# Optimization experiments

Hardware: AMD Instinct MI355X
Metric: run time of the kernel (lower is better)

Reference implementation:

```python
import jax, jax.numpy as jnp
import numpy as np

B, S, IN_DIM, HID = 8, 2048, 1024, 1024


def setup_inputs() -> dict:
    key = jax.random.key(0)
    k1, k2, k3, k4, k5 = jax.random.split(key, 5)
    vec = jax.random.normal(k1, (B, S, IN_DIM), dtype=jnp.float32)
    # nn.Linear-style init scale
    wq_w = jax.random.normal(k2, (HID, IN_DIM), dtype=jnp.float32) / np.sqrt(IN_DIM)
    wq_b = jax.random.normal(k3, (HID,), dtype=jnp.float32) * 0.02
    lin_w = jax.random.normal(k4, (1, HID), dtype=jnp.float32) / np.sqrt(HID)
    lin_b = jax.random.normal(k5, (1,), dtype=jnp.float32) * 0.02
    return {"vec": vec, "wq_w": wq_w, "wq_b": wq_b, "lin_w": lin_w, "lin_b": lin_b}


def reference(vec, wq_w, wq_b, lin_w, lin_b):
    # NOTE: the original forward applies self.wq to BOTH q and k (wk/nq/nk unused).
    q = jnp.einsum('bsi,hi->bsh', vec, wq_w) + wq_b          # [B,S,H]
    ret = jnp.einsum('bsx,bsy->bxy', q, q)                    # [B,H,H] bilinear
    ret = jax.nn.relu(ret)
    out = jnp.einsum('bxy,y->bx', ret, lin_w[0]) + lin_b[0]   # Linear(H,1) -> [B,H]
    return out
```

## Files before the change

kernel.cpp:

```cpp
#include <hip/hip_runtime.h>


#define BM 128
#define BN 128

typedef short     bf16x8 __attribute__((ext_vector_type(8)));
typedef unsigned short u16x8 __attribute__((ext_vector_type(8)));
typedef float     f32x4 __attribute__((ext_vector_type(4)));

__device__ inline unsigned short f2bf(float f) {
  unsigned int u = __float_as_uint(f);
  u += 0x7fffu + ((u >> 16) & 1u);
  return (unsigned short)(u >> 16);
}

__device__ inline u16x8 pack8(float4 a, float4 b) {
  u16x8 r;
  r[0] = f2bf(a.x); r[1] = f2bf(a.y); r[2] = f2bf(a.z); r[3] = f2bf(a.w);
  r[4] = f2bf(b.x); r[5] = f2bf(b.y); r[6] = f2bf(b.z); r[7] = f2bf(b.w);
  return r;
}

__device__ inline void async16(unsigned short* lds, const unsigned short* g) {
  __builtin_amdgcn_global_load_lds(
      (const __attribute__((address_space(1))) void*)g,
      (__attribute__((address_space(3))) void*)lds,
      16, 0, 0);
}

__global__ __launch_bounds__(256) void prep(
    const float* __restrict__ vec, unsigned short* __restrict__ vecbf,
    const float* __restrict__ wq,  unsigned short* __restrict__ wqbf,
    const float* __restrict__ lin_b, float* __restrict__ out)
{
  const int gid = blockIdx.x * 256 + threadIdx.x;
  if (blockIdx.x < 8192) {
    const float4* s = (const float4*)(vec + (size_t)gid * 8);
    float4 a = s[0], b = s[1];
    *(u16x8*)(vecbf + (size_t)gid * 8) = pack8(a, b);
    if (gid < 8192) out[gid] = lin_b[0];
  } else {
    const int i = gid - 8192 * 256;
    const float4* s = (const float4*)(wq + (size_t)i * 8);
    float4 a = s[0], b = s[1];
    *(u16x8*)(wqbf + (size_t)i * 8) = pack8(a, b);
  }
}

__global__ void init_out(float* __restrict__ out, const float* __restrict__ lin_b) {
  int i = blockIdx.x * 256 + threadIdx.x;
  if (i < 8192) out[i] = lin_b[0];
}

__global__ __launch_bounds__(256) void gemm_q(
    const unsigned short* __restrict__ A, const unsigned short* __restrict__ Bm,
    const float* __restrict__ bias, unsigned short* __restrict__ qT)
{
  __shared__ unsigned short As[BM * 32];
  __shared__ unsigned short Bs[BN * 32];

  const int m0 = blockIdx.y * BM;
  const int n0 = blockIdx.x * BN;
  const int t    = threadIdx.x;
  const int lane = t & 63;
  const int wave = t >> 6;
  const int wm = (wave >> 1) * 64;
  const int wn = (wave & 1) * 64;
  const int quad = lane >> 4;
  const int lrow = lane & 15;

  const int srow = t >> 2;
  const int gcol = (((t & 3) ^ ((srow >> 1) & 3)) << 3);
  const unsigned short* gA0 = A  + (size_t)(m0 + srow) * 1024 + gcol;
  const unsigned short* gA1 = gA0 + (size_t)64 * 1024;
  const unsigned short* gB0 = Bm + (size_t)(n0 + srow) * 1024 + gcol;
  const unsigned short* gB1 = gB0 + (size_t)64 * 1024;

  const int rc = (quad ^ ((lrow >> 1) & 3)) << 3;

  f32x4 acc[4][4];
#pragma unroll
  for (int i = 0; i < 4; ++i)
#pragma unroll
    for (int j = 0; j < 4; ++j) acc[i][j] = (f32x4){0.f, 0.f, 0.f, 0.f};

  for (int k0 = 0; k0 < 1024; k0 += 32) {
    async16(&As[t * 8],        gA0 + k0);
    async16(&As[2048 + t * 8], gA1 + k0);
    async16(&Bs[t * 8],        gB0 + k0);
    async16(&Bs[2048 + t * 8], gB1 + k0);
    __syncthreads();

    bf16x8 af[4], bfr[4];
#pragma unroll
    for (int i = 0; i < 4; ++i)
      af[i] = *(const bf16x8*)&As[(wm + i * 16 + lrow) * 32 + rc];
#pragma unroll
    for (int j = 0; j < 4; ++j)
      bfr[j] = *(const bf16x8*)&Bs[(wn + j * 16 + lrow) * 32 + rc];
#pragma unroll
    for (int i = 0; i < 4; ++i)
#pragma unroll
      for (int j = 0; j < 4; ++j)
        acc[i][j] = __builtin_amdgcn_mfma_f32_16x16x32_bf16(af[i], bfr[j], acc[i][j], 0, 0, 0);
    __syncthreads();
  }

#pragma unroll
  for (int i = 0; i < 4; ++i) {
    const int mb = m0 + wm + i * 16 + quad * 4;
#pragma unroll
    for (int r = 0; r < 4; ++r) {
      const float bv = bias[mb + r];
#pragma unroll
      for (int j = 0; j < 4; ++j) {
        const int n = n0 + wn + j * 16 + lrow;
        qT[(size_t)(mb + r) * 16384 + n] = f2bf(acc[i][j][r] + bv);
      }
    }
  }
}

__global__ __launch_bounds__(256) void gemm_q_fused(
    const float* __restrict__ Wq, const float* __restrict__ V,
    const float* __restrict__ bias, unsigned short* __restrict__ qT)
{
  __shared__ unsigned short As[BM * 32];
  __shared__ unsigned short Bs[BN * 32];

  const int m0 = blockIdx.y * BM;
  const int n0 = blockIdx.x * BN;
  const int t    = threadIdx.x;
  const int lane = t & 63;
  const int wave = t >> 6;
  const int wm = (wave >> 1) * 64;
  const int wn = (wave & 1) * 64;
  const int quad = lane >> 4;
  const int lrow = lane & 15;

  const int sr = t >> 1;
  const int sc = (t & 1) << 4;
  const float* gA = Wq + (size_t)(m0 + sr) * 1024 + sc;
  const float* gB = V  + (size_t)(n0 + sr) * 1024 + sc;

  f32x4 acc[4][4];
#pragma unroll
  for (int i = 0; i < 4; ++i)
#pragma unroll
    for (int j = 0; j < 4; ++j) acc[i][j] = (f32x4){0.f, 0.f, 0.f, 0.f};

  for (int k0 = 0; k0 < 1024; k0 += 32) {
    const float4* a4 = (const float4*)(gA + k0);
    const float4* b4 = (const float4*)(gB + k0);
    float4 av0 = a4[0], av1 = a4[1], av2 = a4[2], av3 = a4[3];
    float4 bv0 = b4[0], bv1 = b4[1], bv2 = b4[2], bv3 = b4[3];
    *(u16x8*)&As[sr * 32 + sc]     = pack8(av0, av1);
    *(u16x8*)&As[sr * 32 + sc + 8] = pack8(av2, av3);
    *(u16x8*)&Bs[sr * 32 + sc]     = pack8(bv0, bv1);
    *(u16x8*)&Bs[sr * 32 + sc + 8] = pack8(bv2, bv3);
    __syncthreads();

    bf16x8 af[4], bfr[4];
#pragma unroll
    for (int i = 0; i < 4; ++i)
      af[i] = *(const bf16x8*)&As[(wm + i * 16 + lrow) * 32 + quad * 8];
#pragma unroll
    for (int j = 0; j < 4; ++j)
      bfr[j] = *(const bf16x8*)&Bs[(wn + j * 16 + lrow) * 32 + quad * 8];
#pragma unroll
    for (int i = 0; i < 4; ++i)
#pragma unroll
      for (int j = 0; j < 4; ++j)
        acc[i][j] = __builtin_amdgcn_mfma_f32_16x16x32_bf16(af[i], bfr[j], acc[i][j], 0, 0, 0);
    __syncthreads();
  }

#pragma unroll
  for (int i = 0; i < 4; ++i) {
    const int mb = m0 + wm + i * 16 + quad * 4;
#pragma unroll
    for (int r = 0; r < 4; ++r) {
      const float bv = bias[mb + r];
#pragma unroll
      for (int j = 0; j < 4; ++j) {
        const int n = n0 + wn + j * 16 + lrow;
        qT[(size_t)(mb + r) * 16384 + n] = f2bf(acc[i][j][r] + bv);
      }
    }
  }
}

__global__ __launch_bounds__(256) void syrk_dot(
    const unsigned short* __restrict__ qT, const float* __restrict__ W,
    float* __restrict__ out)
{
  __shared__ unsigned short As[BM * 64];
  __shared__ unsigned short Bs[BN * 64];

  const int bb = blockIdx.z;
  const int job = blockIdx.x;
  int tx = 0;
  while ((tx + 1) * (tx + 2) / 2 <= job) ++tx;
  const int ty = job - tx * (tx + 1) / 2;
  const int x0 = tx * BM;
  const int y0 = ty * BN;
  const bool diag = (tx == ty);

  const int t    = threadIdx.x;
  const int lane = t & 63;
  const int wave = t >> 6;
  const int wm = (wave >> 1) * 64;
  const int wn = (wave & 1) * 64;
  const int quad = lane >> 4;
  const int lrow = lane & 15;

  const int srow = t >> 3;
  const int gcol = (((t & 7) ^ (srow & 7)) << 3);
  const size_t cbase = (size_t)bb * 2048 + gcol;
  const unsigned short* gA = qT + (size_t)(x0 + srow) * 16384 + cbase;
  const unsigned short* gB = qT + (size_t)(y0 + srow) * 16384 + cbase;

  f32x4 acc[4][4];
#pragma unroll
  for (int i = 0; i < 4; ++i)
#pragma unroll
    for (int j = 0; j < 4; ++j) acc[i][j] = (f32x4){0.f, 0.f, 0.f, 0.f};

  for (int k0 = 0; k0 < 2048; k0 += 64) {
#pragma unroll
    for (int p = 0; p < 4; ++p) {
      async16(&As[p * 2048 + t * 8], gA + (size_t)p * 32 * 16384 + k0);
      async16(&Bs[p * 2048 + t * 8], gB + (size_t)p * 32 * 16384 + k0);
    }
    __syncthreads();

#pragma unroll
    for (int kk = 0; kk < 2; ++kk) {
      const int rc = (((kk * 4 + quad) ^ (lrow & 7)) << 3);
      bf16x8 af[4], bfr[4];
#pragma unroll
      for (int i = 0; i < 4; ++i)
        af[i] = *(const bf16x8*)&As[(wm + i * 16 + lrow) * 64 + rc];
#pragma unroll
      for (int j = 0; j < 4; ++j)
        bfr[j] = *(const bf16x8*)&Bs[(wn + j * 16 + lrow) * 64 + rc];
#pragma unroll
      for (int i = 0; i < 4; ++i)
#pragma unroll
        for (int j = 0; j < 4; ++j)
          acc[i][j] = __builtin_amdgcn_mfma_f32_16x16x32_bf16(af[i], bfr[j], acc[i][j], 0, 0, 0);
    }
    __syncthreads();
  }

  float* ob = out + bb * 1024;

  float wv[4];
#pragma unroll
  for (int j = 0; j < 4; ++j) wv[j] = W[y0 + wn + j * 16 + lrow];

#pragma unroll
  for (int i = 0; i < 4; ++i) {
#pragma unroll
    for (int r = 0; r < 4; ++r) {
      float p = 0.f;
#pragma unroll
      for (int j = 0; j < 4; ++j) {
        float v = acc[i][j][r];
        v = v > 0.f ? v : 0.f;
        p += v * wv[j];
      }
#pragma unroll
      for (int off = 1; off < 16; off <<= 1) p += __shfl_xor(p, off, 64);
      if (lrow == 0)
        atomicAdd(&ob[x0 + wm + i * 16 + quad * 4 + r], p);
    }
  }

  if (!diag) {
    float wx[4][4];
#pragma unroll
    for (int i = 0; i < 4; ++i)
#pragma unroll
      for (int r = 0; r < 4; ++r)
        wx[i][r] = W[x0 + wm + i * 16 + quad * 4 + r];

#pragma unroll
    for (int j = 0; j < 4; ++j) {
      float pc = 0.f;
#pragma unroll
      for (int i = 0; i < 4; ++i)
#pragma unroll
        for (int r = 0; r < 4; ++r) {
          float v = acc[i][j][r];
          v = v > 0.f ? v : 0.f;
          pc += v * wx[i][r];
        }
      pc += __shfl_xor(pc, 16, 64);
      pc += __shfl_xor(pc, 32, 64);
      if (quad == 0)
        atomicAdd(&ob[y0 + wn + j * 16 + lrow], pc);
    }
  }
}

extern "C" void kernel_launch(void* const* d_in, const int* in_sizes, int n_in,
                              void* d_out, int out_size, void* d_ws, size_t ws_size,
                              hipStream_t stream) {
  const float* vec   = (const float*)d_in[0];
  const float* wq_w  = (const float*)d_in[1];
  const float* wq_b  = (const float*)d_in[2];
  const float* lin_w = (const float*)d_in[3];
  const float* lin_b = (const float*)d_in[4];
  float* out = (float*)d_out;

  unsigned short* qT = (unsigned short*)d_ws;
  const size_t need = (size_t)(32 + 32 + 2) * 1024 * 1024;

  if (ws_size >= need) {
    unsigned short* vecbf = qT + (size_t)16 * 1024 * 1024;
    unsigned short* wqbf  = vecbf + (size_t)16 * 1024 * 1024;
    prep<<<dim3(8192 + 512), dim3(256), 0, stream>>>(vec, vecbf, wq_w, wqbf, lin_b, out);
    gemm_q<<<dim3(128, 8), dim3(256), 0, stream>>>(wqbf, vecbf, wq_b, qT);
  } else {
    init_out<<<dim3(32), dim3(256), 0, stream>>>(out, lin_b);
    gemm_q_fused<<<dim3(128, 8), dim3(256), 0, stream>>>(wq_w, vec, wq_b, qT);
  }
  syrk_dot<<<dim3(36, 1, 8), dim3(256), 0, stream>>>(qT, lin_w, out);
}
```

Baseline: 186.6 us.

## Rewrite SYRK as single-wave 64x64 tiles with four-stage LDS ring

Replaces the 256-thread, 128x128-tile syrk_dot kernel with a 64-thread, one-wave kernel that computes 64x64 triangular tiles. The K loop is software-pipelined over four LDS buffers: async global-to-LDS loads run three chunks ahead, with no block barriers. The grid grows from 288 to 1088 blocks to spread work across CUs. In exchange, each block uses 64KB of LDS, which limits how many blocks fit per CU, and smaller tiles re-read more of qT. Correctness depends on the compiler inserting the right waits for the LDS DMA loads.

```diff
diff --git a/kernel.cpp b/kernel.cpp
--- a/kernel.cpp
+++ b/kernel.cpp
@@ -21,7 +21,7 @@
   return r;
 }
 
-__device__ inline void async16(unsigned short* lds, const unsigned short* g) {
+__device__ inline void async16(void* lds, const void* g) {
   __builtin_amdgcn_global_load_lds(
       (const __attribute__((address_space(1))) void*)g,
       (__attribute__((address_space(3))) void*)lds,
@@ -190,35 +190,30 @@
   }
 }
 
-__global__ __launch_bounds__(256) void syrk_dot(
+__global__ __launch_bounds__(64) void syrk_wave(
     const unsigned short* __restrict__ qT, const float* __restrict__ W,
     float* __restrict__ out)
 {
-  __shared__ unsigned short As[BM * 64];
-  __shared__ unsigned short Bs[BN * 64];
-
-  const int bb = blockIdx.z;
-  const int job = blockIdx.x;
+  __shared__ unsigned short A0[4096], A1[4096], A2[4096], A3[4096];
+  __shared__ unsigned short B0[4096], B1[4096], B2[4096], B3[4096];
+
+  const int bb  = blockIdx.x & 7;
+  const int job = blockIdx.x >> 3;
   int tx = 0;
   while ((tx + 1) * (tx + 2) / 2 <= job) ++tx;
   const int ty = job - tx * (tx + 1) / 2;
-  const int x0 = tx * BM;
-  const int y0 = ty * BN;
+  const int x0 = tx * 64, y0 = ty * 64;
   const bool diag = (tx == ty);
 
-  const int t    = threadIdx.x;
-  const int lane = t & 63;
-  const int wave = t >> 6;
-  const int wm = (wave >> 1) * 64;
-  const int wn = (wave & 1) * 64;
+  const int lane = threadIdx.x;
   const int quad = lane >> 4;
   const int lrow = lane & 15;
 
-  const int srow = t >> 3;
-  const int gcol = (((t & 7) ^ (srow & 7)) << 3);
-  const size_t cbase = (size_t)bb * 2048 + gcol;
-  const unsigned short* gA = qT + (size_t)(x0 + srow) * 16384 + cbase;
-  const unsigned short* gB = qT + (size_t)(y0 + srow) * 16384 + cbase;
+  const int srow = lane >> 3;
+  const int gch  = (lane & 7) ^ srow;
+  const size_t cb = (size_t)bb * 2048 + gch * 8;
+  const unsigned short* gA = qT + (size_t)(x0 + srow) * 16384 + cb;
+  const unsigned short* gB = qT + (size_t)(y0 + srow) * 16384 + cb;
 
   f32x4 acc[4][4];
 #pragma unroll
@@ -226,38 +221,49 @@
 #pragma unroll
     for (int j = 0; j < 4; ++j) acc[i][j] = (f32x4){0.f, 0.f, 0.f, 0.f};
 
-  for (int k0 = 0; k0 < 2048; k0 += 64) {
-#pragma unroll
-    for (int p = 0; p < 4; ++p) {
-      async16(&As[p * 2048 + t * 8], gA + (size_t)p * 32 * 16384 + k0);
-      async16(&Bs[p * 2048 + t * 8], gB + (size_t)p * 32 * 16384 + k0);
-    }
-    __syncthreads();
-
+  auto stage = [&](int c, unsigned short* Ab, unsigned short* Bb) {
+#pragma unroll
+    for (int p = 0; p < 8; ++p)
+      async16(&Ab[p * 512 + lane * 8], gA + (size_t)p * 8 * 16384 + c * 64);
+#pragma unroll
+    for (int p = 0; p < 8; ++p)
+      async16(&Bb[p * 512 + lane * 8], gB + (size_t)p * 8 * 16384 + c * 64);
+  };
+
+  auto compute = [&](const unsigned short* Ab, const unsigned short* Bb) {
 #pragma unroll
     for (int kk = 0; kk < 2; ++kk) {
-      const int rc = (((kk * 4 + quad) ^ (lrow & 7)) << 3);
+      const int sl = (((kk * 4 + quad) ^ (lrow & 7)) << 3);
       bf16x8 af[4], bfr[4];
 #pragma unroll
       for (int i = 0; i < 4; ++i)
-        af[i] = *(const bf16x8*)&As[(wm + i * 16 + lrow) * 64 + rc];
+        af[i] = *(const bf16x8*)&Ab[(i * 16 + lrow) * 64 + sl];
 #pragma unroll
       for (int j = 0; j < 4; ++j)
-        bfr[j] = *(const bf16x8*)&Bs[(wn + j * 16 + lrow) * 64 + rc];
+        bfr[j] = *(const bf16x8*)&Bb[(j * 16 + lrow) * 64 + sl];
 #pragma unroll
       for (int i = 0; i < 4; ++i)
 #pragma unroll
         for (int j = 0; j < 4; ++j)
           acc[i][j] = __builtin_amdgcn_mfma_f32_16x16x32_bf16(af[i], bfr[j], acc[i][j], 0, 0, 0);
     }
-    __syncthreads();
+  };
+
+  stage(0, A0, B0);
+  stage(1, A1, B1);
+  stage(2, A2, B2);
+  for (int c = 0; c < 32; c += 4) {
+    compute(A0, B0); if (c + 3 < 32) stage(c + 3, A3, B3);
+    compute(A1, B1); if (c + 4 < 32) stage(c + 4, A0, B0);
+    compute(A2, B2); if (c + 5 < 32) stage(c + 5, A1, B1);
+    compute(A3, B3); if (c + 6 < 32) stage(c + 6, A2, B2);
   }
 
   float* ob = out + bb * 1024;
 
   float wv[4];
 #pragma unroll
-  for (int j = 0; j < 4; ++j) wv[j] = W[y0 + wn + j * 16 + lrow];
+  for (int j = 0; j < 4; ++j) wv[j] = W[y0 + j * 16 + lrow];
 
 #pragma unroll
   for (int i = 0; i < 4; ++i) {
@@ -273,7 +279,7 @@
 #pragma unroll
       for (int off = 1; off < 16; off <<= 1) p += __shfl_xor(p, off, 64);
       if (lrow == 0)
-        atomicAdd(&ob[x0 + wm + i * 16 + quad * 4 + r], p);
+        atomicAdd(&ob[x0 + i * 16 + quad * 4 + r], p);
     }
   }
 
@@ -283,7 +289,7 @@
     for (int i = 0; i < 4; ++i)
 #pragma unroll
       for (int r = 0; r < 4; ++r)
-        wx[i][r] = W[x0 + wm + i * 16 + quad * 4 + r];
+        wx[i][r] = W[x0 + i * 16 + quad * 4 + r];
 
 #pragma unroll
     for (int j = 0; j < 4; ++j) {
@@ -299,7 +305,7 @@
       pc += __shfl_xor(pc, 16, 64);
       pc += __shfl_xor(pc, 32, 64);
       if (quad == 0)
-        atomicAdd(&ob[y0 + wn + j * 16 + lrow], pc);
+        atomicAdd(&ob[y0 + j * 16 + lrow], pc);
     }
   }
 }
@@ -326,5 +332,5 @@
     init_out<<<dim3(32), dim3(256), 0, stream>>>(out, lin_b);
     gemm_q_fused<<<dim3(128, 8), dim3(256), 0, stream>>>(wq_w, vec, wq_b, qT);
   }
-  syrk_dot<<<dim3(36, 1, 8), dim3(256), 0, stream>>>(qT, lin_w, out);
-}
+  syrk_wave<<<dim3(136 * 8), dim3(64), 0, stream>>>(qT, lin_w, out);
+}
```

Measured after the change: 218.5 us. 1.17x slower.
